# Performance work log

Hardware: AMD Instinct MI355X
Metric: run time of the kernel (lower is better)

Reference implementation:

```python
import jax, jax.numpy as jnp
import numpy as np

HEADS = 4
HEAD_DIM = 32  # out_features // heads = 128 // 4


def setup_inputs() -> dict:
    key = jax.random.key(0)
    k1, k2, k3, k4 = jax.random.split(key, 4)
    N, IN_F = 200000, 128
    E = 500  # <= 1000 so no edge subsampling; loop covers min(E,500)=all edges
    x = jax.random.normal(k1, (N, IN_F), dtype=jnp.float32)
    edge_index = jax.random.randint(k2, (2, E), 0, N, dtype=jnp.int64)
    # Linear weight [out=heads*head_dim, in] as in torch nn.Linear
    W = jax.random.normal(k3, (HEADS * HEAD_DIM, IN_F), dtype=jnp.float32) * (1.0 / np.sqrt(IN_F))
    a = jax.random.normal(k4, (HEADS, 2 * HEAD_DIM), dtype=jnp.float32) * 0.1
    return {"x": x, "edge_index": edge_index, "W": W, "a": a}


def reference(x, edge_index, W, a):
    N = x.shape[0]
    h = (x @ W.T).reshape(N, HEADS, HEAD_DIM)  # [N, H, D]
    src, dst = edge_index[0], edge_index[1]
    h_src = h[src]  # [E, H, D]
    h_dst = h[dst]  # [E, H, D]
    edge_h = jnp.concatenate([h_src, h_dst], axis=-1)  # [E, H, 2D]
    attn = jnp.sum(edge_h * a, axis=-1)  # [E, H]
    attn = jax.nn.leaky_relu(attn, negative_slope=0.2)
    # out[dst] += 0.1 * attn * h[src], accumulated over duplicate dst
    out = h.at[dst].add(0.1 * attn[:, :, None] * h_src)
    return out.reshape(N, HEADS * HEAD_DIM)  # dropout is identity in eval
```

## Files before the change

### kernel.cpp

```cpp
#include <hip/hip_runtime.h>
#include <hip/hip_bf16.h>


typedef __attribute__((ext_vector_type(8))) short bf16x8;
typedef __attribute__((ext_vector_type(4))) float f32x4;

#define W_PAD 136

__global__ __launch_bounds__(256, 3) void gat_gemm_kernel(
    const float* __restrict__ x,
    const float* __restrict__ W,
    float* __restrict__ out,
    int N) {
  __shared__ __hip_bfloat16 Ws[128 * W_PAD];
  __shared__ __hip_bfloat16 Xs[4][16 * W_PAD];

  const int tid = threadIdx.x;

  #pragma unroll
  for (int it = 0; it < 16; ++it) {
    int seg = tid + it * 256;
    int row = seg >> 5;
    int off = (seg & 31) * 4;
    float4 v = *reinterpret_cast<const float4*>(&W[row * 128 + off]);
    union { ushort4 u4; __hip_bfloat16 h[4]; } wpk;
    wpk.h[0] = __float2bfloat16(v.x);
    wpk.h[1] = __float2bfloat16(v.y);
    wpk.h[2] = __float2bfloat16(v.z);
    wpk.h[3] = __float2bfloat16(v.w);
    *reinterpret_cast<ushort4*>(&Ws[row * W_PAD + off]) = wpk.u4;
  }
  __syncthreads();

  const int wave = tid >> 6;
  const int lane = tid & 63;
  const int m = lane & 15;
  const int q = lane >> 4;

  __hip_bfloat16* xs = &Xs[wave][0];

  const int tiles = N >> 4;
  const int gw = (int)gridDim.x * 4;
  int t = (int)blockIdx.x * 4 + wave;
  if (t >= tiles) return;

  float4 raw[8];
  {
    const float* xt = x + (long)t * 2048;
    #pragma unroll
    for (int i = 0; i < 8; ++i)
      raw[i] = *reinterpret_cast<const float4*>(xt + (i * 64 + lane) * 4);
  }

  while (true) {
    #pragma unroll
    for (int i = 0; i < 8; ++i) {
      int g = i * 64 + lane;
      union { ushort4 u4; __hip_bfloat16 h[4]; } p;
      p.h[0] = __float2bfloat16(raw[i].x);
      p.h[1] = __float2bfloat16(raw[i].y);
      p.h[2] = __float2bfloat16(raw[i].z);
      p.h[3] = __float2bfloat16(raw[i].w);
      *reinterpret_cast<ushort4*>(&xs[(g >> 5) * W_PAD + (g & 31) * 4]) = p.u4;
    }

    const int tn = t + gw;
    if (tn < tiles) {
      const float* xt = x + (long)tn * 2048;
      #pragma unroll
      for (int i = 0; i < 8; ++i)
        raw[i] = *reinterpret_cast<const float4*>(xt + (i * 64 + lane) * 4);
    }

    asm volatile("s_waitcnt lgkmcnt(0)" ::: "memory");
    __builtin_amdgcn_sched_barrier(0);

    bf16x8 af[4];
    #pragma unroll
    for (int s = 0; s < 4; ++s)
      af[s] = *reinterpret_cast<const bf16x8*>(
          &xs[m * W_PAD + s * 32 + q * 8]);

    f32x4 acc[8];
    #pragma unroll
    for (int nt = 0; nt < 8; ++nt) acc[nt] = (f32x4){0.f, 0.f, 0.f, 0.f};
    #pragma unroll
    for (int s = 0; s < 4; ++s) {
      #pragma unroll
      for (int nt = 0; nt < 8; ++nt) {
        bf16x8 wfrag = *reinterpret_cast<const bf16x8*>(
            &Ws[(nt * 16 + m) * W_PAD + s * 32 + q * 8]);
        acc[nt] = __builtin_amdgcn_mfma_f32_16x16x32_bf16(wfrag, af[s],
                                                          acc[nt], 0, 0, 0);
      }
    }

    float* orow = out + (long)(t * 16 + m) * 128 + q * 4;
    #pragma unroll
    for (int nt = 0; nt < 8; ++nt)
      *reinterpret_cast<f32x4*>(orow + nt * 16) = acc[nt];

    if (tn >= tiles) break;
    t = tn;
  }
}

__device__ __forceinline__ int detect_i64(const int* eidx) {
  int or_odd = 0;
  #pragma unroll
  for (int k = 0; k < 16; ++k) or_odd |= eidx[2 * k + 1];
  return or_odd == 0;
}

__global__ __launch_bounds__(128) void gat_edge_attn(
    const int* __restrict__ eidx,
    const float* __restrict__ a,
    const float* __restrict__ h,
    float* __restrict__ contrib,
    int E) {
  const int e = blockIdx.x;
  const int c = threadIdx.x;
  const bool is64 = detect_i64(eidx);
  const int src = is64 ? eidx[2 * e] : eidx[e];
  const int dst = is64 ? eidx[2 * (E + e)] : eidx[E + e];

  const float hs = h[(long)src * 128 + c];
  const float hd = h[(long)dst * 128 + c];

  const int head = c >> 5, d = c & 31;
  float term = a[head * 64 + d] * hs + a[head * 64 + 32 + d] * hd;
  term += __shfl_xor(term, 16);
  term += __shfl_xor(term, 8);
  term += __shfl_xor(term, 4);
  term += __shfl_xor(term, 2);
  term += __shfl_xor(term, 1);
  const float attn = term >= 0.f ? term : 0.2f * term;

  contrib[(long)e * 128 + c] = 0.1f * attn * hs;
}

__global__ __launch_bounds__(128) void gat_edge_scatter(
    const int* __restrict__ eidx,
    const float* __restrict__ contrib,
    float* __restrict__ out,
    int E) {
  const int e = blockIdx.x;
  const int c = threadIdx.x;
  const bool is64 = detect_i64(eidx);
  const int dst = is64 ? eidx[2 * (E + e)] : eidx[E + e];
  atomicAdd(&out[(long)dst * 128 + c], contrib[(long)e * 128 + c]);
}

extern "C" void kernel_launch(void* const* d_in, const int* in_sizes, int n_in,
                              void* d_out, int out_size, void* d_ws, size_t ws_size,
                              hipStream_t stream) {
  const float* x  = (const float*)d_in[0];
  const int* eidx = (const int*)d_in[1];
  const float* W  = (const float*)d_in[2];
  const float* a  = (const float*)d_in[3];
  float* out = (float*)d_out;
  float* contrib = (float*)d_ws;

  const int N = in_sizes[0] / 128;
  const int E = in_sizes[1] / 2;

  const int tiles = N / 16;
  int blocks = (tiles + 3) / 4;
  if (blocks > 768) blocks = 768;
  gat_gemm_kernel<<<blocks, 256, 0, stream>>>(x, W, out, N);
  gat_edge_attn<<<E, 128, 0, stream>>>(eidx, a, out, contrib, E);
  gat_edge_scatter<<<E, 128, 0, stream>>>(eidx, contrib, out, E);
}
```

Before: 193.7 us.

## Load X fragments directly into registers, drop LDS staging, swizzle block order

```diff
diff --git a/kernel.cpp b/kernel.cpp
--- a/kernel.cpp
+++ b/kernel.cpp
@@ -7,13 +7,21 @@
 
 #define W_PAD 136
 
-__global__ __launch_bounds__(256, 3) void gat_gemm_kernel(
+__device__ __forceinline__ bf16x8 pack_bf16x8(float4 v0, float4 v1) {
+  union { bf16x8 v; __hip_bfloat16 h[8]; } u;
+  u.h[0] = __float2bfloat16(v0.x); u.h[1] = __float2bfloat16(v0.y);
+  u.h[2] = __float2bfloat16(v0.z); u.h[3] = __float2bfloat16(v0.w);
+  u.h[4] = __float2bfloat16(v1.x); u.h[5] = __float2bfloat16(v1.y);
+  u.h[6] = __float2bfloat16(v1.z); u.h[7] = __float2bfloat16(v1.w);
+  return u.v;
+}
+
+__global__ __launch_bounds__(256, 4) void gat_gemm_kernel(
     const float* __restrict__ x,
     const float* __restrict__ W,
     float* __restrict__ out,
     int N) {
   __shared__ __hip_bfloat16 Ws[128 * W_PAD];
-  __shared__ __hip_bfloat16 Xs[4][16 * W_PAD];
 
   const int tid = threadIdx.x;
 
@@ -37,49 +45,39 @@
   const int m = lane & 15;
   const int q = lane >> 4;
 
-  __hip_bfloat16* xs = &Xs[wave][0];
+  const int nwg = (int)gridDim.x;
+  const int bid = (int)blockIdx.x;
+  const int swz = (bid & 7) * (nwg >> 3) + (bid >> 3);
 
   const int tiles = N >> 4;
-  const int gw = (int)gridDim.x * 4;
-  int t = (int)blockIdx.x * 4 + wave;
+  const int gw = nwg * 4;
+  int t = swz * 4 + wave;
   if (t >= tiles) return;
 
   float4 raw[8];
   {
-    const float* xt = x + (long)t * 2048;
+    const float* xrow = x + (long)(t * 16 + m) * 128;
     #pragma unroll
-    for (int i = 0; i < 8; ++i)
-      raw[i] = *reinterpret_cast<const float4*>(xt + (i * 64 + lane) * 4);
+    for (int s = 0; s < 4; ++s) {
+      raw[2 * s]     = *reinterpret_cast<const float4*>(xrow + s * 32 + q * 8);
+      raw[2 * s + 1] = *reinterpret_cast<const float4*>(xrow + s * 32 + q * 8 + 4);
+    }
   }
 
   while (true) {
+    bf16x8 af[4];
     #pragma unroll
-    for (int i = 0; i < 8; ++i) {
-      int g = i * 64 + lane;
-      union { ushort4 u4; __hip_bfloat16 h[4]; } p;
-      p.h[0] = __float2bfloat16(raw[i].x);
-      p.h[1] = __float2bfloat16(raw[i].y);
-      p.h[2] = __float2bfloat16(raw[i].z);
-      p.h[3] = __float2bfloat16(raw[i].w);
-      *reinterpret_cast<ushort4*>(&xs[(g >> 5) * W_PAD + (g & 31) * 4]) = p.u4;
-    }
+    for (int s = 0; s < 4; ++s) af[s] = pack_bf16x8(raw[2 * s], raw[2 * s + 1]);
 
     const int tn = t + gw;
     if (tn < tiles) {
-      const float* xt = x + (long)tn * 2048;
+      const float* xrow = x + (long)(tn * 16 + m) * 128;
       #pragma unroll
-      for (int i = 0; i < 8; ++i)
-        raw[i] = *reinterpret_cast<const float4*>(xt + (i * 64 + lane) * 4);
+      for (int s = 0; s < 4; ++s) {
+        raw[2 * s]     = *reinterpret_cast<const float4*>(xrow + s * 32 + q * 8);
+        raw[2 * s + 1] = *reinterpret_cast<const float4*>(xrow + s * 32 + q * 8 + 4);
+      }
     }
-
-    asm volatile("s_waitcnt lgkmcnt(0)" ::: "memory");
-    __builtin_amdgcn_sched_barrier(0);
-
-    bf16x8 af[4];
-    #pragma unroll
-    for (int s = 0; s < 4; ++s)
-      af[s] = *reinterpret_cast<const bf16x8*>(
-          &xs[m * W_PAD + s * 32 + q * 8]);
 
     f32x4 acc[8];
     #pragma unroll
@@ -164,9 +162,7 @@
   const int N = in_sizes[0] / 128;
   const int E = in_sizes[1] / 2;
 
-  const int tiles = N / 16;
-  int blocks = (tiles + 3) / 4;
-  if (blocks > 768) blocks = 768;
+  int blocks = 1024;
   gat_gemm_kernel<<<blocks, 256, 0, stream>>>(x, W, out, N);
   gat_edge_attn<<<E, 128, 0, stream>>>(eidx, a, out, contrib, E);
   gat_edge_scatter<<<E, 128, 0, stream>>>(eidx, contrib, out, E);
```

Measured after the change: 255.7 us. 32.0% more time.

## Share one 16-row X tile per block, split N across waves, swizzle LDS

Applied to the files above, without the earlier changes.

```diff
diff --git a/kernel.cpp b/kernel.cpp
--- a/kernel.cpp
+++ b/kernel.cpp
@@ -5,30 +5,29 @@
 typedef __attribute__((ext_vector_type(8))) short bf16x8;
 typedef __attribute__((ext_vector_type(4))) float f32x4;
 
-#define W_PAD 136
-
-__global__ __launch_bounds__(256, 3) void gat_gemm_kernel(
+__global__ __launch_bounds__(256, 4) void gat_gemm_kernel(
     const float* __restrict__ x,
     const float* __restrict__ W,
     float* __restrict__ out,
     int N) {
-  __shared__ __hip_bfloat16 Ws[128 * W_PAD];
-  __shared__ __hip_bfloat16 Xs[4][16 * W_PAD];
+  __shared__ __align__(16) char WsB[32768];
+  __shared__ __align__(16) char XsB[8192];
 
   const int tid = threadIdx.x;
 
   #pragma unroll
   for (int it = 0; it < 16; ++it) {
-    int seg = tid + it * 256;
+    int seg = it * 256 + tid;
     int row = seg >> 5;
-    int off = (seg & 31) * 4;
-    float4 v = *reinterpret_cast<const float4*>(&W[row * 128 + off]);
+    int o8 = seg & 31;
+    float4 v = *reinterpret_cast<const float4*>(&W[row * 128 + o8 * 4]);
     union { ushort4 u4; __hip_bfloat16 h[4]; } wpk;
     wpk.h[0] = __float2bfloat16(v.x);
     wpk.h[1] = __float2bfloat16(v.y);
     wpk.h[2] = __float2bfloat16(v.z);
     wpk.h[3] = __float2bfloat16(v.w);
-    *reinterpret_cast<ushort4*>(&Ws[row * W_PAD + off]) = wpk.u4;
+    *reinterpret_cast<ushort4*>(
+        WsB + row * 256 + ((o8 * 8) ^ ((row & 7) << 4))) = wpk.u4;
   }
   __syncthreads();
 
@@ -37,70 +36,91 @@
   const int m = lane & 15;
   const int q = lane >> 4;
 
-  __hip_bfloat16* xs = &Xs[wave][0];
+  const int T16 = N >> 4;
+  const int stride = (int)gridDim.x;
+  int t = (int)blockIdx.x;
 
-  const int tiles = N >> 4;
-  const int gw = (int)gridDim.x * 4;
-  int t = (int)blockIdx.x * 4 + wave;
-  if (t >= tiles) return;
-
-  float4 raw[8];
+  float4 raw[2];
   {
     const float* xt = x + (long)t * 2048;
     #pragma unroll
-    for (int i = 0; i < 8; ++i)
-      raw[i] = *reinterpret_cast<const float4*>(xt + (i * 64 + lane) * 4);
+    for (int i = 0; i < 2; ++i)
+      raw[i] = *reinterpret_cast<const float4*>(xt + (i * 256 + tid) * 4);
   }
 
   while (true) {
     #pragma unroll
-    for (int i = 0; i < 8; ++i) {
-      int g = i * 64 + lane;
+    for (int i = 0; i < 2; ++i) {
+      int g = i * 256 + tid;
       union { ushort4 u4; __hip_bfloat16 h[4]; } p;
       p.h[0] = __float2bfloat16(raw[i].x);
       p.h[1] = __float2bfloat16(raw[i].y);
       p.h[2] = __float2bfloat16(raw[i].z);
       p.h[3] = __float2bfloat16(raw[i].w);
-      *reinterpret_cast<ushort4*>(&xs[(g >> 5) * W_PAD + (g & 31) * 4]) = p.u4;
+      int row = g >> 5, o8 = g & 31;
+      *reinterpret_cast<ushort4*>(
+          XsB + row * 256 + ((o8 * 8) ^ ((row & 7) << 4))) = p.u4;
     }
 
-    const int tn = t + gw;
-    if (tn < tiles) {
+    const int tn = t + stride;
+    if (tn < T16) {
       const float* xt = x + (long)tn * 2048;
       #pragma unroll
-      for (int i = 0; i < 8; ++i)
-        raw[i] = *reinterpret_cast<const float4*>(xt + (i * 64 + lane) * 4);
+      for (int i = 0; i < 2; ++i)
+        raw[i] = *reinterpret_cast<const float4*>(xt + (i * 256 + tid) * 4);
     }
 
     asm volatile("s_waitcnt lgkmcnt(0)" ::: "memory");
     __builtin_amdgcn_sched_barrier(0);
+    __builtin_amdgcn_s_barrier();
 
     bf16x8 af[4];
     #pragma unroll
     for (int s = 0; s < 4; ++s)
       af[s] = *reinterpret_cast<const bf16x8*>(
-          &xs[m * W_PAD + s * 32 + q * 8]);
+          XsB + m * 256 + ((s * 64 + q * 16) ^ ((m & 7) << 4)));
 
-    f32x4 acc[8];
-    #pragma unroll
-    for (int nt = 0; nt < 8; ++nt) acc[nt] = (f32x4){0.f, 0.f, 0.f, 0.f};
+    f32x4 acc[2];
+    acc[0] = (f32x4){0.f, 0.f, 0.f, 0.f};
+    acc[1] = (f32x4){0.f, 0.f, 0.f, 0.f};
     #pragma unroll
     for (int s = 0; s < 4; ++s) {
       #pragma unroll
-      for (int nt = 0; nt < 8; ++nt) {
+      for (int k = 0; k < 2; ++k) {
+        const int nt = 2 * wave + k;
         bf16x8 wfrag = *reinterpret_cast<const bf16x8*>(
-            &Ws[(nt * 16 + m) * W_PAD + s * 32 + q * 8]);
-        acc[nt] = __builtin_amdgcn_mfma_f32_16x16x32_bf16(wfrag, af[s],
-                                                          acc[nt], 0, 0, 0);
+            WsB + (nt * 16 + m) * 256 + ((s * 64 + q * 16) ^ ((m & 7) << 4)));
+        acc[k] = __builtin_amdgcn_mfma_f32_16x16x32_bf16(wfrag, af[s],
+                                                         acc[k], 0, 0, 0);
       }
     }
 
-    float* orow = out + (long)(t * 16 + m) * 128 + q * 4;
+    __builtin_amdgcn_s_barrier();
+
     #pragma unroll
-    for (int nt = 0; nt < 8; ++nt)
-      *reinterpret_cast<f32x4*>(orow + nt * 16) = acc[nt];
+    for (int k = 0; k < 2; ++k)
+      *reinterpret_cast<f32x4*>(
+          XsB + m * 512 +
+          (((2 * wave + k) * 64 + q * 16) ^ ((m & 7) << 4))) = acc[k];
 
-    if (tn >= tiles) break;
+    asm volatile("s_waitcnt lgkmcnt(0)" ::: "memory");
+    __builtin_amdgcn_sched_barrier(0);
+    __builtin_amdgcn_s_barrier();
+
+    {
+      char* ob = (char*)out + (long)t * 8192;
+      #pragma unroll
+      for (int i = 0; i < 2; ++i) {
+        int g = i * 256 + tid;
+        f32x4 v = *reinterpret_cast<const f32x4*>(
+            XsB + (g >> 5) * 512 + (((g & 31) * 16) ^ (((g >> 5) & 7) << 4)));
+        *reinterpret_cast<f32x4*>(ob + g * 16) = v;
+      }
+    }
+
+    __builtin_amdgcn_s_barrier();
+
+    if (tn >= T16) break;
     t = tn;
   }
 }
@@ -164,9 +184,7 @@
   const int N = in_sizes[0] / 128;
   const int E = in_sizes[1] / 2;
 
-  const int tiles = N / 16;
-  int blocks = (tiles + 3) / 4;
-  if (blocks > 768) blocks = 768;
+  int blocks = 1024;
   gat_gemm_kernel<<<blocks, 256, 0, stream>>>(x, W, out, N);
   gat_edge_attn<<<E, 128, 0, stream>>>(eidx, a, out, contrib, E);
   gat_edge_scatter<<<E, 128, 0, stream>>>(eidx, contrib, out, E);
```

New measurement: 192.3 us. About the same (-0.7%).
